# Performance work log

Measured on AMD Instinct MI355X. Metric: run time of the kernel, lower is better.

The kernel has to match this reference:

```python
import jax, jax.numpy as jnp
import numpy as np

NUM_EMBEDDINGS = 4096
EMBEDDING_DIM = 128
COMMITMENT_COST = 0.25


def setup_inputs() -> dict:
    key = jax.random.key(0)
    k_x, k_w = jax.random.split(key)
    inputs = jax.random.normal(k_x, (32, 128, 32, 32), dtype=jnp.float32)
    # xavier_uniform for Embedding weight [K, D]: bound = sqrt(6/(K+D))
    bound = float(np.sqrt(6.0 / (NUM_EMBEDDINGS + EMBEDDING_DIM)))
    weight = jax.random.uniform(k_w, (NUM_EMBEDDINGS, EMBEDDING_DIM),
                                dtype=jnp.float32, minval=-bound, maxval=bound)
    return {"inputs": inputs, "weight": weight}


def reference(inputs, weight):
    K, D = weight.shape
    # channels-first 4D input with C == embedding_dim -> NHWC
    x = jnp.transpose(inputs, (0, 2, 3, 1))  # [B, H, W, D]
    input_shape = x.shape
    flat = x.reshape(-1, D)                  # [N, D]

    x_sq = jnp.sum(flat * flat, axis=1, keepdims=True)          # [N, 1]
    w_sq = jnp.sum(weight * weight, axis=1)                     # [K]
    two_xy = 2.0 * jnp.matmul(flat, weight.T)                   # [N, K]
    distances = x_sq - two_xy + w_sq[None, :] + 1e-8

    encoding_indices = jnp.argmin(distances, axis=1)            # [N] int

    quantized = weight[encoding_indices].reshape(input_shape)   # [B, H, W, D]

    q_latent_loss = jnp.mean((quantized - x) ** 2)
    e_latent_loss = jnp.mean((jax.lax.stop_gradient(quantized) - x) ** 2)
    loss = q_latent_loss + COMMITMENT_COST * e_latent_loss
    loss = jnp.where(jnp.isnan(loss) | jnp.isinf(loss), jnp.float32(0.1), loss)

    quantized_st = x + jax.lax.stop_gradient(quantized - x)

    counts = jnp.zeros((K,), dtype=jnp.float32).at[encoding_indices].add(1.0)
    avg_probs = counts / encoding_indices.shape[0]
    perplexity = jnp.exp(-jnp.sum(avg_probs * jnp.log(avg_probs + 1e-10)))

    encodings = jax.nn.one_hot(encoding_indices, K, dtype=jnp.float32)  # [N, K]

    # input was channels-first -> restore NCHW
    quantized_st = jnp.transpose(quantized_st, (0, 3, 1, 2))
    return quantized_st, loss, perplexity, encodings, encoding_indices
```

## Files before the change

### kernel.cpp

```cpp
#include <hip/hip_runtime.h>
#include <stdint.h>
#include <math.h>

#define K_CODES 4096
#define DIM 128
#define N_FLAT 32768
#define HW 1024

#define OFF_Q    0
#define OFF_LOSS 4194304
#define OFF_PERP 4194305
#define OFF_ENC  4194306
#define OFF_IDX  138412034

#define WS_PACKED 0
#define WS_COUNTS 262144
#define WS_WSQ    278528
#define WS_XSQ    294912
#define WS_PART   425984
#define WS_XHL    430080
#define WS_WHL    (WS_XHL + 16777216)

typedef _Float16 f16x8 __attribute__((ext_vector_type(8)));
typedef float    f32x4 __attribute__((ext_vector_type(4)));


__global__ __launch_bounds__(256) void wsq_kernel(const float* __restrict__ w,
                                                  float* __restrict__ wsq,
                                                  float* __restrict__ counts) {
    int wave = threadIdx.x >> 6, lane = threadIdx.x & 63;
    int k = blockIdx.x * 4 + wave;
    float a = w[k * DIM + lane];
    float b = w[k * DIM + lane + 64];
    float s = a * a + b * b;
    #pragma unroll
    for (int o = 32; o > 0; o >>= 1) s += __shfl_down(s, o, 64);
    if (lane == 0) { wsq[k] = s; counts[k] = 0.f; }
}

__global__ __launch_bounds__(256) void wplanes_kernel(const float* __restrict__ w,
                                                      _Float16* __restrict__ whl) {
    int T = blockIdx.x * 256 + threadIdx.x;
    int k = T >> 2, seg = T & 3;
    const float* wp = w + (size_t)k * DIM + seg * 32;
    _Float16* row = whl + (size_t)k * 256;
    #pragma unroll
    for (int q = 0; q < 4; ++q) {
        float4 a = *(const float4*)(wp + q * 8);
        float4 b = *(const float4*)(wp + q * 8 + 4);
        float vv[8] = {a.x, a.y, a.z, a.w, b.x, b.y, b.z, b.w};
        f16x8 hv, lv;
        #pragma unroll
        for (int j = 0; j < 8; ++j) {
            float v = 1024.0f * vv[j];
            _Float16 h = (_Float16)v;
            _Float16 l = (_Float16)(v - (float)h);
            hv[j] = h; lv[j] = l;
        }
        *(f16x8*)(row + seg * 32 + q * 8) = hv;
        *(f16x8*)(row + 128 + seg * 32 + q * 8) = lv;
    }
}

__global__ __launch_bounds__(256) void xprep_kernel(const float* __restrict__ x,
                                                    _Float16* __restrict__ xhl,
                                                    float* __restrict__ xsq,
                                                    unsigned long long* __restrict__ packed) {
    __shared__ float xt[128 * 65];
    const int t = threadIdx.x;
    const int n0 = blockIdx.x * 64;
    const int b = n0 >> 10, hw0 = n0 & 1023;
    const float* xg = x + (size_t)b * (DIM * HW) + hw0;
    #pragma unroll
    for (int i = 0; i < 16; ++i) {
        int idx = i * 256 + t;
        int c = idx >> 5, n2 = (idx & 31) << 1;
        float2 v = *(const float2*)(xg + c * HW + n2);
        xt[c * 65 + n2] = v.x;
        xt[c * 65 + n2 + 1] = v.y;
    }
    __syncthreads();
    if (t < 64) {
        packed[n0 + t] = ~0ull;
        float s = 0.f;
        #pragma unroll
        for (int c = 0; c < DIM; ++c) {
            float v = xt[c * 65 + t];
            s = fmaf(v, v, s);
        }
        xsq[n0 + t] = s;
    }
    const int n = t >> 2, seg = t & 3;
    _Float16* row = xhl + (size_t)(n0 + n) * 256;
    #pragma unroll
    for (int q = 0; q < 4; ++q) {
        f16x8 hv, lv;
        #pragma unroll
        for (int j = 0; j < 8; ++j) {
            float v = 32.0f * xt[(seg * 32 + q * 8 + j) * 65 + n];
            _Float16 h = (_Float16)v;
            _Float16 l = (_Float16)(v - (float)h);
            hv[j] = h; lv[j] = l;
        }
        *(f16x8*)(row + seg * 32 + q * 8) = hv;
        *(f16x8*)(row + 128 + seg * 32 + q * 8) = lv;
    }
}

__global__ __launch_bounds__(256) void dist_argmin(
    const _Float16* __restrict__ xhl, const _Float16* __restrict__ whl,
    const float* __restrict__ wsq, const float* __restrict__ xsq,
    unsigned long long* __restrict__ packed, float* __restrict__ enc)
{
    __shared__ __align__(16) _Float16 xl[128 * 72];
    __shared__ __align__(16) _Float16 wl[128 * 72];
    __shared__ float xsq_s[128], wsq_s[128];
    __shared__ unsigned long long red[128][2];

    const int tid  = threadIdx.x;
    const int lane = tid & 63, wave = tid >> 6;
    const int lq   = lane & 15, quad = lane >> 4;
    const int wn0  = (wave >> 1) * 64, wk0 = (wave & 1) * 64;
    const int n0   = blockIdx.x * 128;
    const int kbase = blockIdx.y * 512;

    const int sr = tid >> 3, sh = (tid >> 2) & 1, sq = tid & 3;

    {
        float* ebase = enc + (size_t)n0 * K_CODES + kbase;
        float4 z4; z4.x = z4.y = z4.z = z4.w = 0.f;
        #pragma unroll 8
        for (int i = 0; i < 64; ++i) {
            int idx = i * 256 + tid;
            int r = idx >> 7, c4 = idx & 127;
            *(float4*)(ebase + (size_t)r * K_CODES + 2 + c4 * 4) = z4;
        }
        if (tid < 128) {
            float2 z2; z2.x = 0.f; z2.y = 0.f;
            *(float2*)(ebase + (size_t)tid * K_CODES) = z2;
        }
    }

    if (tid < 128) xsq_s[tid] = xsq[n0 + tid];

    const _Float16* xbase = xhl + (size_t)n0 * 256;

    for (int ks = 0; ks < 4; ++ks) {
        const int k0 = kbase + ks * 128;
        if (tid < 128) wsq_s[tid] = wsq[k0 + tid];
        const _Float16* wbase = whl + (size_t)k0 * 256;

        f32x4 acc[4][4];
        #pragma unroll
        for (int i = 0; i < 4; ++i)
            #pragma unroll
            for (int j = 0; j < 4; ++j)
                acc[i][j] = (f32x4){0.f, 0.f, 0.f, 0.f};

        #pragma unroll
        for (int c0 = 0; c0 < 4; ++c0) {
            __syncthreads();
            #pragma unroll
            for (int i = 0; i < 4; ++i) {
                int r = sr + i * 32;
                int goff = r * 256 + sh * 128 + c0 * 32 + sq * 8;
                int loff = r * 72 + sh * 32 + sq * 8;
                *(f16x8*)(xl + loff) = *(const f16x8*)(xbase + goff);
                *(f16x8*)(wl + loff) = *(const f16x8*)(wbase + goff);
            }
            __syncthreads();

            f16x8 ah[4], al[4], bh[4], bl[4];
            #pragma unroll
            for (int i = 0; i < 4; ++i) {
                int xrow = (wn0 + i * 16 + lq) * 72 + quad * 8;
                ah[i] = *(const f16x8*)(xl + xrow);
                al[i] = *(const f16x8*)(xl + xrow + 32);
                int wrow = (wk0 + i * 16 + lq) * 72 + quad * 8;
                bh[i] = *(const f16x8*)(wl + wrow);
                bl[i] = *(const f16x8*)(wl + wrow + 32);
            }
            #pragma unroll
            for (int ki = 0; ki < 4; ++ki)
                #pragma unroll
                for (int ni = 0; ni < 4; ++ni) {
                    acc[ni][ki] = __builtin_amdgcn_mfma_f32_16x16x32_f16(
                        ah[ni], bh[ki], acc[ni][ki], 0, 0, 0);
                    acc[ni][ki] = __builtin_amdgcn_mfma_f32_16x16x32_f16(
                        ah[ni], bl[ki], acc[ni][ki], 0, 0, 0);
                    acc[ni][ki] = __builtin_amdgcn_mfma_f32_16x16x32_f16(
                        al[ni], bh[ki], acc[ni][ki], 0, 0, 0);
                }
        }

        #pragma unroll
        for (int ni = 0; ni < 4; ++ni) {
            #pragma unroll
            for (int rg = 0; rg < 4; ++rg) {
                int rowl = wn0 + ni * 16 + quad * 4 + rg;
                float xr = xsq_s[rowl];
                float best = 3.4e38f; int bk = 0;
                #pragma unroll
                for (int ki = 0; ki < 4; ++ki) {
                    int kl = wk0 + ki * 16 + lq;
                    float t = xr - acc[ni][ki][rg] * 6.103515625e-05f;
                    t += wsq_s[kl];
                    t += 1e-8f;
                    if (t < best) { best = t; bk = k0 + kl; }
                }
                unsigned u = __float_as_uint(best);
                u = (u & 0x80000000u) ? ~u : (u | 0x80000000u);
                unsigned long long p =
                    ((unsigned long long)u << 32) | (unsigned)bk;
                #pragma unroll
                for (int m = 1; m < 16; m <<= 1) {
                    unsigned long long o = __shfl_xor(p, m, 64);
                    if (o < p) p = o;
                }
                if (lq == 0) red[rowl][wave & 1] = p;
            }
        }
        __syncthreads();
        if (tid < 128) {
            unsigned long long a = red[tid][0], b = red[tid][1];
            atomicMin(&packed[n0 + tid], a < b ? a : b);
        }
    }
}

__global__ __launch_bounds__(256) void combine(
    const unsigned long long* __restrict__ packed,
    float* __restrict__ idxf, float* __restrict__ enc,
    float* __restrict__ counts)
{
    int n = blockIdx.x * 256 + threadIdx.x;
    unsigned k = (unsigned)(packed[n] & 0xFFFFFFFFu);
    idxf[n] = (float)k;
    enc[(size_t)n * K_CODES + k] = 1.0f;
    atomicAdd(&counts[k], 1.0f);
}

__global__ __launch_bounds__(256) void quantize_loss(
    const float* __restrict__ x, const float* __restrict__ w,
    const float* __restrict__ idxf, float* __restrict__ outq,
    float* __restrict__ part)
{
    const int base4 = (blockIdx.x * 256 + threadIdx.x) * 4;
    float s = 0.f;
    #pragma unroll
    for (int i = 0; i < 4; ++i) {
        int e  = base4 + i * 1048576;
        int hw = e & 1023;
        int c  = (e >> 10) & 127;
        int b  = e >> 17;
        int n  = (b << 10) | hw;
        float4 xv = *(const float4*)(x + e);
        float4 kf = *(const float4*)(idxf + n);
        float q0 = w[(int)kf.x * DIM + c];
        float q1 = w[(int)kf.y * DIM + c];
        float q2 = w[(int)kf.z * DIM + c];
        float q3 = w[(int)kf.w * DIM + c];
        float4 df; df.x = q0 - xv.x; df.y = q1 - xv.y;
                   df.z = q2 - xv.z; df.w = q3 - xv.w;
        float4 o;  o.x = xv.x + df.x; o.y = xv.y + df.y;
                   o.z = xv.z + df.z; o.w = xv.w + df.w;
        *(float4*)(outq + e) = o;
        s = fmaf(df.x, df.x, s);
        s = fmaf(df.y, df.y, s);
        s = fmaf(df.z, df.z, s);
        s = fmaf(df.w, df.w, s);
    }
    #pragma unroll
    for (int o = 32; o > 0; o >>= 1) s += __shfl_down(s, o, 64);
    __shared__ float ls[4];
    if ((threadIdx.x & 63) == 0) ls[threadIdx.x >> 6] = s;
    __syncthreads();
    if (threadIdx.x == 0) part[blockIdx.x] = ls[0] + ls[1] + ls[2] + ls[3];
}

__global__ __launch_bounds__(256) void finalize(
    const float* __restrict__ counts, const float* __restrict__ part,
    float* __restrict__ out)
{
    __shared__ float sh[512];
    float h = 0.f;
    for (int k = threadIdx.x; k < K_CODES; k += 256) {
        float p = counts[k] * (1.0f / N_FLAT);
        h += p * logf(p + 1e-10f);
    }
    float s = 0.f;
    for (int i = threadIdx.x; i < 1024; i += 256) s += part[i];
    sh[threadIdx.x] = h;
    sh[256 + threadIdx.x] = s;
    __syncthreads();
    #pragma unroll
    for (int st = 128; st > 0; st >>= 1) {
        if (threadIdx.x < st) {
            sh[threadIdx.x] += sh[threadIdx.x + st];
            sh[256 + threadIdx.x] += sh[256 + threadIdx.x + st];
        }
        __syncthreads();
    }
    if (threadIdx.x == 0) {
        float perp = expf(-sh[0]);
        float loss = 1.25f * (sh[256] / 4194304.0f);
        if (isnan(loss) || isinf(loss)) loss = 0.1f;
        out[OFF_LOSS] = loss;
        out[OFF_PERP] = perp;
    }
}

extern "C" void kernel_launch(void* const* d_in, const int* in_sizes, int n_in,
                              void* d_out, int out_size, void* d_ws, size_t ws_size,
                              hipStream_t stream) {
    const float* x = (const float*)d_in[0];
    const float* w = (const float*)d_in[1];
    float* out = (float*)d_out;
    char* ws = (char*)d_ws;

    unsigned long long* packed = (unsigned long long*)(ws + WS_PACKED);
    float* counts = (float*)(ws + WS_COUNTS);
    float* wsq    = (float*)(ws + WS_WSQ);
    float* xsq    = (float*)(ws + WS_XSQ);
    float* part   = (float*)(ws + WS_PART);
    _Float16* xhl = (_Float16*)(ws + WS_XHL);
    _Float16* whl = (_Float16*)(ws + WS_WHL);

    wsq_kernel<<<K_CODES / 4, 256, 0, stream>>>(w, wsq, counts);
    wplanes_kernel<<<K_CODES * 4 / 256, 256, 0, stream>>>(w, whl);
    xprep_kernel<<<N_FLAT / 64, 256, 0, stream>>>(x, xhl, xsq, packed);

    dim3 g2(256, 8);
    dist_argmin<<<g2, 256, 0, stream>>>(xhl, whl, wsq, xsq, packed,
                                        out + OFF_ENC);

    combine<<<N_FLAT / 256, 256, 0, stream>>>(packed, out + OFF_IDX,
                                              out + OFF_ENC, counts);

    quantize_loss<<<1024, 256, 0, stream>>>(x, w, out + OFF_IDX,
                                            out + OFF_Q, part);

    finalize<<<1, 256, 0, stream>>>(counts, part, out);
}
```

Measured before the change: 845.2 us.

## Interleave encoding zero-fill with GEMM and defer argmin reduction to kernel end

Spreads the one-hot zero-fill stores across the k-loop iterations so they overlap MFMA work instead of running as an up-front burst. Keeps a per-thread running best across the four k-subtiles and performs the shuffle reduction and atomicMin once at the end rather than per subtile. Reads codebook norms from global into registers instead of through shared memory, and adds a launch-bounds occupancy hint of 3 blocks. This holds 16 extra 64-bit values per thread, which raises register pressure and may conflict with the occupancy target.

```diff
diff --git a/kernel.cpp b/kernel.cpp
--- a/kernel.cpp
+++ b/kernel.cpp
@@ -107,14 +107,14 @@
     }
 }
 
-__global__ __launch_bounds__(256) void dist_argmin(
+__global__ __launch_bounds__(256, 3) void dist_argmin(
     const _Float16* __restrict__ xhl, const _Float16* __restrict__ whl,
     const float* __restrict__ wsq, const float* __restrict__ xsq,
     unsigned long long* __restrict__ packed, float* __restrict__ enc)
 {
     __shared__ __align__(16) _Float16 xl[128 * 72];
     __shared__ __align__(16) _Float16 wl[128 * 72];
-    __shared__ float xsq_s[128], wsq_s[128];
+    __shared__ float xsq_s[128];
     __shared__ unsigned long long red[128][2];
 
     const int tid  = threadIdx.x;
@@ -124,31 +124,32 @@
     const int n0   = blockIdx.x * 128;
     const int kbase = blockIdx.y * 512;
 
-    const int sr = tid >> 3, sh = (tid >> 2) & 1, sq = tid & 3;
-
-    {
-        float* ebase = enc + (size_t)n0 * K_CODES + kbase;
-        float4 z4; z4.x = z4.y = z4.z = z4.w = 0.f;
-        #pragma unroll 8
-        for (int i = 0; i < 64; ++i) {
-            int idx = i * 256 + tid;
-            int r = idx >> 7, c4 = idx & 127;
-            *(float4*)(ebase + (size_t)r * K_CODES + 2 + c4 * 4) = z4;
-        }
-        if (tid < 128) {
-            float2 z2; z2.x = 0.f; z2.y = 0.f;
-            *(float2*)(ebase + (size_t)tid * K_CODES) = z2;
-        }
-    }
-
-    if (tid < 128) xsq_s[tid] = xsq[n0 + tid];
+    const int sr = tid >> 3, shh = (tid >> 2) & 1, sq = tid & 3;
+
+    float* ebase = enc + (size_t)n0 * K_CODES + kbase;
+    if (tid < 128) {
+        float2 z2; z2.x = 0.f; z2.y = 0.f;
+        *(float2*)(ebase + (size_t)tid * K_CODES) = z2;
+        xsq_s[tid] = xsq[n0 + tid];
+    }
 
     const _Float16* xbase = xhl + (size_t)n0 * 256;
+
+    unsigned long long pbest[4][4];
+    #pragma unroll
+    for (int i = 0; i < 4; ++i)
+        #pragma unroll
+        for (int j = 0; j < 4; ++j)
+            pbest[i][j] = ~0ull;
 
     for (int ks = 0; ks < 4; ++ks) {
         const int k0 = kbase + ks * 128;
-        if (tid < 128) wsq_s[tid] = wsq[k0 + tid];
         const _Float16* wbase = whl + (size_t)k0 * 256;
+
+        float wk[4];
+        #pragma unroll
+        for (int ki = 0; ki < 4; ++ki)
+            wk[ki] = wsq[k0 + wk0 + ki * 16 + lq];
 
         f32x4 acc[4][4];
         #pragma unroll
@@ -163,10 +164,20 @@
             #pragma unroll
             for (int i = 0; i < 4; ++i) {
                 int r = sr + i * 32;
-                int goff = r * 256 + sh * 128 + c0 * 32 + sq * 8;
-                int loff = r * 72 + sh * 32 + sq * 8;
+                int goff = r * 256 + shh * 128 + c0 * 32 + sq * 8;
+                int loff = r * 72 + shh * 32 + sq * 8;
                 *(f16x8*)(xl + loff) = *(const f16x8*)(xbase + goff);
                 *(f16x8*)(wl + loff) = *(const f16x8*)(wbase + goff);
+            }
+            {
+                int batch = ks * 4 + c0;
+                float4 z4; z4.x = z4.y = z4.z = z4.w = 0.f;
+                #pragma unroll
+                for (int j = 0; j < 4; ++j) {
+                    int idx = batch * 1024 + j * 256 + tid;
+                    int r = idx >> 7, c4 = idx & 127;
+                    *(float4*)(ebase + (size_t)r * K_CODES + 2 + c4 * 4) = z4;
+                }
             }
             __syncthreads();
 
@@ -204,7 +215,7 @@
                 for (int ki = 0; ki < 4; ++ki) {
                     int kl = wk0 + ki * 16 + lq;
                     float t = xr - acc[ni][ki][rg] * 6.103515625e-05f;
-                    t += wsq_s[kl];
+                    t += wk[ki];
                     t += 1e-8f;
                     if (t < best) { best = t; bk = k0 + kl; }
                 }
@@ -212,19 +223,28 @@
                 u = (u & 0x80000000u) ? ~u : (u | 0x80000000u);
                 unsigned long long p =
                     ((unsigned long long)u << 32) | (unsigned)bk;
-                #pragma unroll
-                for (int m = 1; m < 16; m <<= 1) {
-                    unsigned long long o = __shfl_xor(p, m, 64);
-                    if (o < p) p = o;
-                }
-                if (lq == 0) red[rowl][wave & 1] = p;
-            }
-        }
-        __syncthreads();
-        if (tid < 128) {
-            unsigned long long a = red[tid][0], b = red[tid][1];
-            atomicMin(&packed[n0 + tid], a < b ? a : b);
-        }
+                if (p < pbest[ni][rg]) pbest[ni][rg] = p;
+            }
+        }
+    }
+
+    #pragma unroll
+    for (int ni = 0; ni < 4; ++ni) {
+        #pragma unroll
+        for (int rg = 0; rg < 4; ++rg) {
+            unsigned long long p = pbest[ni][rg];
+            #pragma unroll
+            for (int m = 1; m < 16; m <<= 1) {
+                unsigned long long o = __shfl_xor(p, m, 64);
+                if (o < p) p = o;
+            }
+            if (lq == 0) red[wn0 + ni * 16 + quad * 4 + rg][wave & 1] = p;
+        }
+    }
+    __syncthreads();
+    if (tid < 128) {
+        unsigned long long a = red[tid][0], b = red[tid][1];
+        atomicMin(&packed[n0 + tid], a < b ? a : b);
     }
 }
 
```

New measurement: 879.5 us. 1.04x slower.

## Keep x tile resident in swizzled LDS and stream codebook via registers

Applied to the files above, without the earlier changes.

The distance/argmin kernel now loads the block's whole 128-row x tile (hi+lo halves) once into XOR-swizzled shared memory and reads codebook fragments straight from global memory into registers, double-buffered so the next chunk is prefetched during the MFMAs. This removes the per-chunk __syncthreads pairs and LDS staging of W. The zero-fill of the one-hot encodings is spread across the compute steps to overlap stores with math. The per-ks reductions are folded into a shared atomicMin, with one global atomic per row at the end. The 64KB LDS buffer and launch_bounds(256,2) may limit occupancy and raise register pressure.

```diff
diff --git a/kernel.cpp b/kernel.cpp
--- a/kernel.cpp
+++ b/kernel.cpp
@@ -107,15 +107,14 @@
     }
 }
 
-__global__ __launch_bounds__(256) void dist_argmin(
+__global__ __launch_bounds__(256, 2) void dist_argmin(
     const _Float16* __restrict__ xhl, const _Float16* __restrict__ whl,
     const float* __restrict__ wsq, const float* __restrict__ xsq,
     unsigned long long* __restrict__ packed, float* __restrict__ enc)
 {
-    __shared__ __align__(16) _Float16 xl[128 * 72];
-    __shared__ __align__(16) _Float16 wl[128 * 72];
-    __shared__ float xsq_s[128], wsq_s[128];
-    __shared__ unsigned long long red[128][2];
+    __shared__ __align__(16) char xs[128 * 512];
+    __shared__ float xsq_s[128];
+    __shared__ unsigned long long red[128];
 
     const int tid  = threadIdx.x;
     const int lane = tid & 63, wave = tid >> 6;
@@ -123,75 +122,98 @@
     const int wn0  = (wave >> 1) * 64, wk0 = (wave & 1) * 64;
     const int n0   = blockIdx.x * 128;
     const int kbase = blockIdx.y * 512;
-
-    const int sr = tid >> 3, sh = (tid >> 2) & 1, sq = tid & 3;
-
-    {
-        float* ebase = enc + (size_t)n0 * K_CODES + kbase;
-        float4 z4; z4.x = z4.y = z4.z = z4.w = 0.f;
-        #pragma unroll 8
-        for (int i = 0; i < 64; ++i) {
-            int idx = i * 256 + tid;
-            int r = idx >> 7, c4 = idx & 127;
-            *(float4*)(ebase + (size_t)r * K_CODES + 2 + c4 * 4) = z4;
-        }
-        if (tid < 128) {
-            float2 z2; z2.x = 0.f; z2.y = 0.f;
-            *(float2*)(ebase + (size_t)tid * K_CODES) = z2;
-        }
-    }
-
-    if (tid < 128) xsq_s[tid] = xsq[n0 + tid];
+    const int swz  = (lq & 7) << 4;
+
+    float* ebase = enc + (size_t)n0 * K_CODES + kbase;
+    float* efill = ebase + (size_t)(tid >> 7) * K_CODES + 2 + (tid & 127) * 4;
+
+    if (tid < 128) {
+        float2 z2; z2.x = 0.f; z2.y = 0.f;
+        *(float2*)(ebase + (size_t)tid * K_CODES) = z2;
+        xsq_s[tid] = xsq[n0 + tid];
+        red[tid] = ~0ull;
+    }
 
     const _Float16* xbase = xhl + (size_t)n0 * 256;
+    #pragma unroll
+    for (int i = 0; i < 16; ++i) {
+        int idx = i * 256 + tid;
+        int r  = idx >> 5;
+        int bc = (idx & 31) << 4;
+        f16x8 v = *(const f16x8*)(xbase + idx * 8);
+        *(f16x8*)(xs + r * 512 + (bc ^ ((r & 7) << 4))) = v;
+    }
+    __syncthreads();
+
+    const _Float16* wrow = whl + (size_t)(kbase + wk0 + lq) * 256 + quad * 8;
+    int rowb[4];
+    #pragma unroll
+    for (int i = 0; i < 4; ++i) rowb[i] = (wn0 + i * 16 + lq) * 512;
+
+    f32x4 acc[4][4];
+    float wk[4];
+    f16x8 bhA[4], blA[4], bhB[4], blB[4];
+
+    #pragma unroll
+    for (int ki = 0; ki < 4; ++ki) {
+        bhA[ki] = *(const f16x8*)(wrow + ki * 4096);
+        blA[ki] = *(const f16x8*)(wrow + ki * 4096 + 128);
+    }
+
+#define STEP(ks_, c0_, CH, CL, PRE, PH, PL, preoff_)                          \
+    do {                                                                       \
+        f16x8 ah[4], al[4];                                                    \
+        _Pragma("unroll")                                                      \
+        for (int i = 0; i < 4; ++i) {                                          \
+            int cb = (c0_) * 64 + quad * 16;                                   \
+            ah[i] = *(const f16x8*)(xs + rowb[i] + (cb ^ swz));                \
+            al[i] = *(const f16x8*)(xs + rowb[i] + 256 + (cb ^ swz));          \
+        }                                                                      \
+        if (PRE) {                                                             \
+            _Pragma("unroll")                                                  \
+            for (int ki = 0; ki < 4; ++ki) {                                   \
+                PH[ki] = *(const f16x8*)(wrow + (preoff_) + ki * 4096);        \
+                PL[ki] = *(const f16x8*)(wrow + (preoff_) + ki * 4096 + 128);  \
+            }                                                                  \
+        }                                                                      \
+        {                                                                      \
+            float4 z4; z4.x = z4.y = z4.z = z4.w = 0.f;                        \
+            const int s_ = (ks_) * 4 + (c0_);                                  \
+            _Pragma("unroll")                                                  \
+            for (int j = 0; j < 4; ++j)                                        \
+                *(float4*)(efill + (size_t)(s_ * 8 + j * 2) * K_CODES) = z4;   \
+        }                                                                      \
+        _Pragma("unroll")                                                      \
+        for (int ki = 0; ki < 4; ++ki)                                         \
+            _Pragma("unroll")                                                  \
+            for (int ni = 0; ni < 4; ++ni) {                                   \
+                acc[ni][ki] = __builtin_amdgcn_mfma_f32_16x16x32_f16(          \
+                    ah[ni], CH[ki], acc[ni][ki], 0, 0, 0);                     \
+                acc[ni][ki] = __builtin_amdgcn_mfma_f32_16x16x32_f16(          \
+                    ah[ni], CL[ki], acc[ni][ki], 0, 0, 0);                     \
+                acc[ni][ki] = __builtin_amdgcn_mfma_f32_16x16x32_f16(          \
+                    al[ni], CH[ki], acc[ni][ki], 0, 0, 0);                     \
+            }                                                                  \
+    } while (0)
 
     for (int ks = 0; ks < 4; ++ks) {
         const int k0 = kbase + ks * 128;
-        if (tid < 128) wsq_s[tid] = wsq[k0 + tid];
-        const _Float16* wbase = whl + (size_t)k0 * 256;
-
-        f32x4 acc[4][4];
+        #pragma unroll
+        for (int ki = 0; ki < 4; ++ki)
+            wk[ki] = wsq[k0 + wk0 + ki * 16 + lq];
         #pragma unroll
         for (int i = 0; i < 4; ++i)
             #pragma unroll
             for (int j = 0; j < 4; ++j)
                 acc[i][j] = (f32x4){0.f, 0.f, 0.f, 0.f};
 
-        #pragma unroll
-        for (int c0 = 0; c0 < 4; ++c0) {
-            __syncthreads();
-            #pragma unroll
-            for (int i = 0; i < 4; ++i) {
-                int r = sr + i * 32;
-                int goff = r * 256 + sh * 128 + c0 * 32 + sq * 8;
-                int loff = r * 72 + sh * 32 + sq * 8;
-                *(f16x8*)(xl + loff) = *(const f16x8*)(xbase + goff);
-                *(f16x8*)(wl + loff) = *(const f16x8*)(wbase + goff);
-            }
-            __syncthreads();
-
-            f16x8 ah[4], al[4], bh[4], bl[4];
-            #pragma unroll
-            for (int i = 0; i < 4; ++i) {
-                int xrow = (wn0 + i * 16 + lq) * 72 + quad * 8;
-                ah[i] = *(const f16x8*)(xl + xrow);
-                al[i] = *(const f16x8*)(xl + xrow + 32);
-                int wrow = (wk0 + i * 16 + lq) * 72 + quad * 8;
-                bh[i] = *(const f16x8*)(wl + wrow);
-                bl[i] = *(const f16x8*)(wl + wrow + 32);
-            }
-            #pragma unroll
-            for (int ki = 0; ki < 4; ++ki)
-                #pragma unroll
-                for (int ni = 0; ni < 4; ++ni) {
-                    acc[ni][ki] = __builtin_amdgcn_mfma_f32_16x16x32_f16(
-                        ah[ni], bh[ki], acc[ni][ki], 0, 0, 0);
-                    acc[ni][ki] = __builtin_amdgcn_mfma_f32_16x16x32_f16(
-                        ah[ni], bl[ki], acc[ni][ki], 0, 0, 0);
-                    acc[ni][ki] = __builtin_amdgcn_mfma_f32_16x16x32_f16(
-                        al[ni], bh[ki], acc[ni][ki], 0, 0, 0);
-                }
-        }
+        const int wko = ks * 32768;
+
+        STEP(ks, 0, bhA, blA, 1, bhB, blB, wko + 32);
+        STEP(ks, 1, bhB, blB, 1, bhA, blA, wko + 64);
+        STEP(ks, 2, bhA, blA, 1, bhB, blB, wko + 96);
+        if (ks < 3) STEP(ks, 3, bhB, blB, 1, bhA, blA, wko + 32768);
+        else        STEP(ks, 3, bhB, blB, 0, bhA, blA, 0);
 
         #pragma unroll
         for (int ni = 0; ni < 4; ++ni) {
@@ -204,28 +226,27 @@
                 for (int ki = 0; ki < 4; ++ki) {
                     int kl = wk0 + ki * 16 + lq;
                     float t = xr - acc[ni][ki][rg] * 6.103515625e-05f;
-                    t += wsq_s[kl];
+                    t += wk[ki];
                     t += 1e-8f;
                     if (t < best) { best = t; bk = k0 + kl; }
                 }
                 unsigned u = __float_as_uint(best);
                 u = (u & 0x80000000u) ? ~u : (u | 0x80000000u);
-                unsigned long long p =
+                unsigned long long pck =
                     ((unsigned long long)u << 32) | (unsigned)bk;
                 #pragma unroll
                 for (int m = 1; m < 16; m <<= 1) {
-                    unsigned long long o = __shfl_xor(p, m, 64);
-                    if (o < p) p = o;
+                    unsigned long long o = __shfl_xor(pck, m, 64);
+                    if (o < pck) pck = o;
                 }
-                if (lq == 0) red[rowl][wave & 1] = p;
+                if (lq == 0) atomicMin(&red[rowl], pck);
             }
         }
-        __syncthreads();
-        if (tid < 128) {
-            unsigned long long a = red[tid][0], b = red[tid][1];
-            atomicMin(&packed[n0 + tid], a < b ? a : b);
-        }
-    }
+    }
+#undef STEP
+
+    __syncthreads();
+    if (tid < 128) atomicMin(&packed[n0 + tid], red[tid]);
 }
 
 __global__ __launch_bounds__(256) void combine(
```

After: 940.0 us. 11.2% more time.
